# Kernel optimization log

Hardware: AMD Instinct MI355X
Metric: run time of the kernel (lower is better)

## Reference

```python
import jax, jax.numpy as jnp
import numpy as np

EPS = 1e-06
NEG_SLOPE = 0.2
B, N, CIN = 2, 2048, 64
QK, V, H = 128, 128, 8


def ev_nonlin(x, w1, b1, w2, b2):
    # EVNNonLinearity with skip_connection == 1, leaky_relu
    norm = jnp.linalg.norm(x, axis=-2, keepdims=True)  # [..., 1, nf]
    zero_norm = norm <= EPS
    norm = norm + EPS
    h = jax.nn.leaky_relu(norm @ w1 + b1, NEG_SLOPE)
    norm_bn = (h @ w2 + b2) + norm
    return jnp.where(zero_norm, x, x / norm * norm_bn)


def ev_layernorm(x):
    x_norm = jnp.linalg.norm(x, axis=-2, keepdims=True)
    sigma = jnp.std(jnp.concatenate([x_norm, -x_norm], -1), axis=-1, keepdims=True)
    return x / (sigma + EPS)


def setup_inputs() -> dict:
    key = jax.random.key(0)
    ks = jax.random.split(key, 20)
    def w(k, *shape):
        fan_in = shape[0]
        return jax.random.normal(k, shape, jnp.float32) / np.sqrt(fan_in)
    hd_qk = QK // H
    hd_v = V // H
    return {
        'qfts': jax.random.normal(ks[0], (B, N, 3, CIN), jnp.float32),
        'kvfts': jax.random.normal(ks[1], (B, N, 3, CIN), jnp.float32),
        # EVLinearLeakyReLU for q branch
        'w_q_in': w(ks[2], CIN, QK),
        'q_nl_w1': w(ks[3], QK, QK // 2), 'q_nl_b1': jnp.zeros((QK // 2,), jnp.float32),
        'q_nl_w2': w(ks[4], QK // 2, QK), 'q_nl_b2': jnp.zeros((QK,), jnp.float32),
        # EVLinearLeakyReLU for kv branch
        'w_kv_in': w(ks[5], CIN, QK),
        'kv_nl_w1': w(ks[6], QK, QK // 2), 'kv_nl_b1': jnp.zeros((QK // 2,), jnp.float32),
        'kv_nl_w2': w(ks[7], QK // 2, QK), 'kv_nl_b2': jnp.zeros((QK,), jnp.float32),
        # DenseGeneral projections (no bias)
        'w_q': w(ks[8], QK, H, hd_qk),
        'w_k': w(ks[9], QK, H, hd_qk),
        'w_v': w(ks[10], QK, H, hd_v),
        # output EVLinearLeakyReLU
        'w_out': w(ks[11], V, V),
        'o_nl_w1': w(ks[12], V, V // 2), 'o_nl_b1': jnp.zeros((V // 2,), jnp.float32),
        'o_nl_w2': w(ks[13], V // 2, V), 'o_nl_b2': jnp.zeros((V,), jnp.float32),
    }


def reference(qfts, kvfts, w_q_in, q_nl_w1, q_nl_b1, q_nl_w2, q_nl_b2,
              w_kv_in, kv_nl_w1, kv_nl_b1, kv_nl_w2, kv_nl_b2,
              w_q, w_k, w_v, w_out, o_nl_w1, o_nl_b1, o_nl_w2, o_nl_b2):
    # EVLinearLeakyReLU on q and kv features: [b,n,3,cin] -> [b,n,3,qk]
    qf = ev_nonlin(qfts @ w_q_in, q_nl_w1, q_nl_b1, q_nl_w2, q_nl_b2)
    kf = ev_nonlin(kvfts @ w_kv_in, kv_nl_w1, kv_nl_b1, kv_nl_w2, kv_nl_b2)
    # DenseGeneral to heads, then heads to front: [h,b,n,3,d]
    q = jnp.einsum('bnfc,chd->hbnfd', qf, w_q)
    k = jnp.einsum('bnfc,chd->hbnfd', kf, w_k)
    v = jnp.einsum('bnfc,chd->hbnfd', kf, w_v)
    # normalize_qk
    q = ev_layernorm(q)
    k = ev_layernorm(k)
    # dot attention: contract vector(3) and head_dim axes
    scale = np.sqrt(k.shape[-1]).astype(np.float32)
    attn = jnp.einsum('hbqfd,hbkfd->hbqk', q, k)
    attn = jax.nn.softmax(attn / scale, axis=-1)
    resi = jnp.einsum('hbqk,hbkfd->hbqfd', attn, v)
    # 'h b q f d -> b q f (h d)'
    h, b, nq, f, d = resi.shape
    resi = jnp.moveaxis(resi, 0, 3).reshape(b, nq, f, h * d)
    # output EVLinearLeakyReLU
    out = ev_nonlin(resi @ w_out, o_nl_w1, o_nl_b1, o_nl_w2, o_nl_b2)
    return out
```

## Files before the change

kernel.cpp:

```cpp
#include <hip/hip_runtime.h>
#include <math.h>

#define EPSV 1e-6f
#define NSL  0.2f
#define BB   2
#define NN   2048
#define HH   8
#define TBP  16

typedef short bf16x8 __attribute__((ext_vector_type(8)));
typedef float f32x4  __attribute__((ext_vector_type(4)));

__device__ __forceinline__ unsigned cvt_pk_bf16(float a, float b) {
  unsigned r;
  asm("v_cvt_pk_bf16_f32 %0, %1, %2" : "=v"(r) : "v"(a), "v"(b));
  return r;
}
__device__ __forceinline__ float u2f(unsigned u) {
  union { unsigned u; float f; } v; v.u = u; return v.f;
}
__device__ __forceinline__ float leaky(float a) { return a > 0.f ? a : NSL * a; }

__device__ __forceinline__ void pack8(float4 a, float4 b, uint4& hi, uint4& lo) {
  hi.x = cvt_pk_bf16(a.x, a.y);
  hi.y = cvt_pk_bf16(a.z, a.w);
  hi.z = cvt_pk_bf16(b.x, b.y);
  hi.w = cvt_pk_bf16(b.z, b.w);
  float d0 = a.x - u2f(hi.x << 16), d1 = a.y - u2f(hi.x & 0xffff0000u);
  float d2 = a.z - u2f(hi.y << 16), d3 = a.w - u2f(hi.y & 0xffff0000u);
  float d4 = b.x - u2f(hi.z << 16), d5 = b.y - u2f(hi.z & 0xffff0000u);
  float d6 = b.z - u2f(hi.w << 16), d7 = b.w - u2f(hi.w & 0xffff0000u);
  lo.x = cvt_pk_bf16(d0, d1);
  lo.y = cvt_pk_bf16(d2, d3);
  lo.z = cvt_pk_bf16(d4, d5);
  lo.w = cvt_pk_bf16(d6, d7);
}

__global__ __launch_bounds__(64) void wconv_kernel(
    const float* __restrict__ wq_in, const float* __restrict__ qw1, const float* __restrict__ qw2,
    const float* __restrict__ wkv_in, const float* __restrict__ kw1, const float* __restrict__ kw2,
    const float* __restrict__ w_q, const float* __restrict__ w_k, const float* __restrict__ w_v,
    unsigned short* __restrict__ WB)
{
  const int b = blockIdx.x;
  const int lane = threadIdx.x;
  const float* src; int N, toff;
  if      (b < 16)  { src = wq_in;  N = 128; toff = b; }
  else if (b < 32)  { src = qw1;    N = 64;  toff = b - 16; }
  else if (b < 48)  { src = qw2;    N = 128; toff = b - 32; }
  else if (b < 64)  { src = wkv_in; N = 128; toff = b - 48; }
  else if (b < 80)  { src = kw1;    N = 64;  toff = b - 64; }
  else if (b < 96)  { src = kw2;    N = 128; toff = b - 80; }
  else if (b < 128) { src = w_q;    N = 128; toff = b - 96; }
  else if (b < 160) { src = w_k;    N = 128; toff = b - 128; }
  else              { src = w_v;    N = 128; toff = b - 160; }
  const int NT = N >> 4;
  const int kk = toff / NT, nj = toff % NT;
  const int k0 = kk * 32 + (lane >> 4) * 8;
  const int ch = nj * 16 + (lane & 15);
  float vals[8];
  #pragma unroll
  for (int j = 0; j < 8; ++j) vals[j] = src[(size_t)(k0 + j) * N + ch];
  float4 a = {vals[0], vals[1], vals[2], vals[3]};
  float4 bb = {vals[4], vals[5], vals[6], vals[7]};
  uint4 hi, lo;
  pack8(a, bb, hi, lo);
  unsigned short* dst = WB + (size_t)b * 1024;
  *(uint4*)(dst + lane * 8) = hi;
  *(uint4*)(dst + 512 + lane * 8) = lo;
}


__global__ __launch_bounds__(256) void pre_kernel(
    const float* __restrict__ qfts, const float* __restrict__ kvfts,
    const float* __restrict__ qb1, const float* __restrict__ qb2,
    const float* __restrict__ kb1, const float* __restrict__ kb2,
    const unsigned short* __restrict__ WB,
    unsigned short* __restrict__ QW, unsigned short* __restrict__ KW, unsigned short* __restrict__ VW)
{
  const bool is_kv = blockIdx.y != 0;
  const float* x_in = is_kv ? kvfts : qfts;
  const float* b1 = is_kv ? kb1 : qb1;
  const float* b2 = is_kv ? kb2 : qb2;
  unsigned short* FW = is_kv ? KW : QW;
  const float ln_sc = is_kv ? 1.f : 0.25f * 1.44269504088896f;
  const int tb_in = is_kv ? 48 : 0;
  const int tb_w1 = is_kv ? 64 : 16;
  const int tb_w2 = is_kv ? 80 : 32;
  const int tb_p  = is_kv ? 128 : 96;

  const int t0 = blockIdx.x * TBP;
  const int tid = threadIdx.x;
  const int wv = tid >> 6, lane = tid & 63;
  const int col = lane & 15, kg = lane >> 4;
  const int nj0 = wv * 2;
  const int n0 = t0 & (NN - 1), bsel = t0 >> 11;

  __shared__ __align__(16) char smem[50688];
  float* xs       = (float*)smem;
  float* norm_lds = (float*)(smem + 12544);
  float* h_lds    = (float*)(smem + 20992);
  float* f_lds    = (float*)(smem + 25344);
  float* stage    = (float*)smem;

  {
    const float4* src = (const float4*)(x_in + (size_t)t0 * 192);
    #pragma unroll
    for (int i = 0; i < 3; ++i) {
      int idx = tid + i * 256;
      int row = idx / 48, c4 = idx % 48;
      *(float4*)&xs[row * 196 + c4 * 4] = src[idx];
    }
  }
  __syncthreads();

  f32x4 pacc[3][2];
  #pragma unroll
  for (int mf = 0; mf < 3; ++mf)
    #pragma unroll
    for (int njl = 0; njl < 2; ++njl) pacc[mf][njl] = (f32x4){0.f, 0.f, 0.f, 0.f};
  {
    bf16x8 axh[3][2], axl[3][2];
    #pragma unroll
    for (int mf = 0; mf < 3; ++mf)
      #pragma unroll
      for (int kk = 0; kk < 2; ++kk) {
        const float* pa = &xs[col * 196 + mf * 64 + kk * 32 + kg * 8];
        uint4 hi, lo;
        pack8(*(const float4*)pa, *(const float4*)(pa + 4), hi, lo);
        axh[mf][kk] = *(bf16x8*)&hi; axl[mf][kk] = *(bf16x8*)&lo;
      }
    #pragma unroll
    for (int kk = 0; kk < 2; ++kk)
      #pragma unroll
      for (int njl = 0; njl < 2; ++njl) {
        const unsigned short* wb = WB + (size_t)(tb_in + kk * 8 + nj0 + njl) * 1024 + lane * 8;
        bf16x8 bh = *(const bf16x8*)wb;
        bf16x8 bl = *(const bf16x8*)(wb + 512);
        #pragma unroll
        for (int mf = 0; mf < 3; ++mf) {
          pacc[mf][njl] = __builtin_amdgcn_mfma_f32_16x16x32_bf16(axh[mf][kk], bh, pacc[mf][njl], 0, 0, 0);
          pacc[mf][njl] = __builtin_amdgcn_mfma_f32_16x16x32_bf16(axh[mf][kk], bl, pacc[mf][njl], 0, 0, 0);
          pacc[mf][njl] = __builtin_amdgcn_mfma_f32_16x16x32_bf16(axl[mf][kk], bh, pacc[mf][njl], 0, 0, 0);
        }
      }
  }

  f32x4 np4[2]; int zm = 0;
  #pragma unroll
  for (int njl = 0; njl < 2; ++njl) {
    f32x4 ss = pacc[0][njl] * pacc[0][njl] + pacc[1][njl] * pacc[1][njl] + pacc[2][njl] * pacc[2][njl];
    #pragma unroll
    for (int i = 0; i < 4; ++i) {
      float nn = sqrtf(ss[i]);
      if (nn <= EPSV) zm |= 1 << (njl * 4 + i);
      np4[njl][i] = nn + EPSV;
      norm_lds[(kg * 4 + i) * 132 + (nj0 + njl) * 16 + col] = np4[njl][i];
    }
  }
  __syncthreads();

  {
    f32x4 hacc = {0.f, 0.f, 0.f, 0.f};
    #pragma unroll
    for (int kk = 0; kk < 4; ++kk) {
      const float* pa = &norm_lds[col * 132 + kk * 32 + kg * 8];
      uint4 hi, lo;
      pack8(*(const float4*)pa, *(const float4*)(pa + 4), hi, lo);
      bf16x8 ah = *(bf16x8*)&hi, al = *(bf16x8*)&lo;
      const unsigned short* wb = WB + (size_t)(tb_w1 + kk * 4 + wv) * 1024 + lane * 8;
      bf16x8 bh = *(const bf16x8*)wb, bl = *(const bf16x8*)(wb + 512);
      hacc = __builtin_amdgcn_mfma_f32_16x16x32_bf16(ah, bh, hacc, 0, 0, 0);
      hacc = __builtin_amdgcn_mfma_f32_16x16x32_bf16(ah, bl, hacc, 0, 0, 0);
      hacc = __builtin_amdgcn_mfma_f32_16x16x32_bf16(al, bh, hacc, 0, 0, 0);
    }
    float b1v = b1[wv * 16 + col];
    #pragma unroll
    for (int i = 0; i < 4; ++i)
      h_lds[(kg * 4 + i) * 68 + wv * 16 + col] = leaky(hacc[i] + b1v);
  }
  __syncthreads();

  {
    f32x4 bna[2] = {{0.f, 0.f, 0.f, 0.f}, {0.f, 0.f, 0.f, 0.f}};
    #pragma unroll
    for (int kk = 0; kk < 2; ++kk) {
      const float* pa = &h_lds[col * 68 + kk * 32 + kg * 8];
      uint4 hi, lo;
      pack8(*(const float4*)pa, *(const float4*)(pa + 4), hi, lo);
      bf16x8 ah = *(bf16x8*)&hi, al = *(bf16x8*)&lo;
      #pragma unroll
      for (int njl = 0; njl < 2; ++njl) {
        const unsigned short* wb = WB + (size_t)(tb_w2 + kk * 8 + nj0 + njl) * 1024 + lane * 8;
        bf16x8 bh = *(const bf16x8*)wb, bl = *(const bf16x8*)(wb + 512);
        bna[njl] = __builtin_amdgcn_mfma_f32_16x16x32_bf16(ah, bh, bna[njl], 0, 0, 0);
        bna[njl] = __builtin_amdgcn_mfma_f32_16x16x32_bf16(ah, bl, bna[njl], 0, 0, 0);
        bna[njl] = __builtin_amdgcn_mfma_f32_16x16x32_bf16(al, bh, bna[njl], 0, 0, 0);
      }
    }
    #pragma unroll
    for (int njl = 0; njl < 2; ++njl) {
      float b2v = b2[(nj0 + njl) * 16 + col];
      #pragma unroll
      for (int i = 0; i < 4; ++i) {
        float r = (zm >> (njl * 4 + i)) & 1 ? 1.f
                 : (bna[njl][i] + b2v + np4[njl][i]) / np4[njl][i];
        #pragma unroll
        for (int mf = 0; mf < 3; ++mf)
          f_lds[(mf * 16 + kg * 4 + i) * 132 + (nj0 + njl) * 16 + col] = pacc[mf][njl][i] * r;
      }
    }
  }
  __syncthreads();

  f32x4 qacc[3][2], vacc[3][2];
  #pragma unroll
  for (int mf = 0; mf < 3; ++mf)
    #pragma unroll
    for (int njl = 0; njl < 2; ++njl) {
      qacc[mf][njl] = (f32x4){0.f, 0.f, 0.f, 0.f};
      vacc[mf][njl] = (f32x4){0.f, 0.f, 0.f, 0.f};
    }
  #pragma unroll
  for (int kk = 0; kk < 4; ++kk) {
    bf16x8 afh[3], afl[3];
    #pragma unroll
    for (int mf = 0; mf < 3; ++mf) {
      const float* pa = &f_lds[(mf * 16 + col) * 132 + kk * 32 + kg * 8];
      uint4 hi, lo;
      pack8(*(const float4*)pa, *(const float4*)(pa + 4), hi, lo);
      afh[mf] = *(bf16x8*)&hi; afl[mf] = *(bf16x8*)&lo;
    }
    #pragma unroll
    for (int njl = 0; njl < 2; ++njl) {
      const unsigned short* wbq = WB + (size_t)(tb_p + kk * 8 + nj0 + njl) * 1024 + lane * 8;
      bf16x8 qbh = *(const bf16x8*)wbq, qbl = *(const bf16x8*)(wbq + 512);
      #pragma unroll
      for (int mf = 0; mf < 3; ++mf) {
        qacc[mf][njl] = __builtin_amdgcn_mfma_f32_16x16x32_bf16(afh[mf], qbh, qacc[mf][njl], 0, 0, 0);
        qacc[mf][njl] = __builtin_amdgcn_mfma_f32_16x16x32_bf16(afh[mf], qbl, qacc[mf][njl], 0, 0, 0);
        qacc[mf][njl] = __builtin_amdgcn_mfma_f32_16x16x32_bf16(afl[mf], qbh, qacc[mf][njl], 0, 0, 0);
      }
      if (is_kv) {
        const unsigned short* wbv = WB + (size_t)(160 + kk * 8 + nj0 + njl) * 1024 + lane * 8;
        bf16x8 vbh = *(const bf16x8*)wbv, vbl = *(const bf16x8*)(wbv + 512);
        #pragma unroll
        for (int mf = 0; mf < 3; ++mf) {
          vacc[mf][njl] = __builtin_amdgcn_mfma_f32_16x16x32_bf16(afh[mf], vbh, vacc[mf][njl], 0, 0, 0);
          vacc[mf][njl] = __builtin_amdgcn_mfma_f32_16x16x32_bf16(afh[mf], vbl, vacc[mf][njl], 0, 0, 0);
          vacc[mf][njl] = __builtin_amdgcn_mfma_f32_16x16x32_bf16(afl[mf], vbh, vacc[mf][njl], 0, 0, 0);
        }
      }
    }
  }
  __syncthreads();

  #pragma unroll
  for (int njl = 0; njl < 2; ++njl) {
    #pragma unroll
    for (int i = 0; i < 4; ++i) {
      float ss = qacc[0][njl][i] * qacc[0][njl][i]
               + qacc[1][njl][i] * qacc[1][njl][i]
               + qacc[2][njl][i] * qacc[2][njl][i];
      ss += __shfl_xor(ss, 1, 16);
      ss += __shfl_xor(ss, 2, 16);
      ss += __shfl_xor(ss, 4, 16);
      ss += __shfl_xor(ss, 8, 16);
      float inv = ln_sc / (sqrtf(ss * (1.f / 16.f)) + EPSV);
      const int tl = kg * 4 + i;
      #pragma unroll
      for (int mf = 0; mf < 3; ++mf)
        stage[tl * 388 + mf * 128 + (nj0 + njl) * 16 + col] = qacc[mf][njl][i] * inv;
    }
  }
  __syncthreads();

  {
    const int f0 = lane >> 5;
    const int ddb = ((lane >> 4) & 1) * 8;
    const int row = lane & 15;
    #pragma unroll
    for (int h2 = 0; h2 < 2; ++h2) {
      const int hh = wv * 2 + h2;
      const int hbw = hh * BB + bsel;
      const size_t basew = (size_t)(hbw * 128 + (n0 >> 4)) * 1536;
      {
        const float* p0 = stage + row * 388 + f0 * 128 + hh * 16 + ddb;
        uint4 hi, lo;
        pack8(*(const float4*)p0, *(const float4*)(p0 + 4), hi, lo);
        *(uint4*)(FW + basew + lane * 8) = hi;
        *(uint4*)(FW + basew + 768 + lane * 8) = lo;
      }
      if (lane < 32) {
        const float* p1 = stage + row * 388 + 2 * 128 + hh * 16 + ddb;
        uint4 hi, lo;
        pack8(*(const float4*)p1, *(const float4*)(p1 + 4), hi, lo);
        *(uint4*)(FW + basew + 512 + lane * 8) = hi;
        *(uint4*)(FW + basew + 768 + 512 + lane * 8) = lo;
      }
    }
  }

  if (is_kv) {
    __syncthreads();
    #pragma unroll
    for (int njl = 0; njl < 2; ++njl)
      #pragma unroll
      for (int mf = 0; mf < 3; ++mf)
        #pragma unroll
        for (int i = 0; i < 4; ++i)
          stage[mf * 2112 + (kg * 4 + i) * 132 + (nj0 + njl) * 16 + col] = vacc[mf][njl][i];
    __syncthreads();

    const int s0 = (n0 >> 3) & 3;
    if (lane < 32) {
      const int seg = lane;
      const int tlb = (seg >> 4) * 8;
      const int dd = seg & 15;
      #pragma unroll
      for (int h2 = 0; h2 < 2; ++h2) {
        const int hh = wv * 2 + h2;
        const int hbw = hh * BB + bsel;
        #pragma unroll
        for (int f = 0; f < 3; ++f) {
          const size_t vbase = (size_t)((hbw * 64 + (n0 >> 5)) * 3 + f) * 1024;
          float vals[8];
          #pragma unroll
          for (int j = 0; j < 8; ++j)
            vals[j] = stage[f * 2112 + (tlb + j) * 132 + hh * 16 + dd];
          float4 a = {vals[0], vals[1], vals[2], vals[3]};
          float4 b = {vals[4], vals[5], vals[6], vals[7]};
          uint4 hi, lo;
          pack8(a, b, hi, lo);
          *(uint4*)(VW + vbase + (size_t)(s0 * 16 + seg) * 8) = hi;
          *(uint4*)(VW + vbase + 512 + (size_t)(s0 * 16 + seg) * 8) = lo;
        }
      }
    }
  }
}

#define THR 10.0f

__global__ __launch_bounds__(512, 4) void attn_kernel(
    const unsigned short* __restrict__ QW, const unsigned short* __restrict__ KW,
    const unsigned short* __restrict__ VW, float* __restrict__ Ob)
{
  const int lane = threadIdx.x & 63;
  const int w = threadIdx.x >> 6;
  const int qt = w & 1;
  const int kq = w >> 1;
  const int hb = blockIdx.y;
  const int tA = blockIdx.x * 4 + qt * 2;
  const int q = lane & 15, g = lane >> 4;

  __shared__ unsigned short plds[8][2][1152];
  float* comb = (float*)plds;

  bf16x8 qh0[2], ql0[2], qh1[2], ql1[2];
  #pragma unroll
  for (int qs = 0; qs < 2; ++qs) {
    const size_t qbase = (size_t)(hb * 128 + tA + qs) * 1536;
    qh0[qs] = *(const bf16x8*)(QW + qbase + lane * 8);
    ql0[qs] = *(const bf16x8*)(QW + qbase + 768 + lane * 8);
    qh1[qs] = (bf16x8){0,0,0,0,0,0,0,0};
    ql1[qs] = (bf16x8){0,0,0,0,0,0,0,0};
    if (lane < 32) {
      qh1[qs] = *(const bf16x8*)(QW + qbase + 512 + lane * 8);
      ql1[qs] = *(const bf16x8*)(QW + qbase + 768 + 512 + lane * 8);
    }
  }

  f32x4 o[2][3];
  #pragma unroll
  for (int qs = 0; qs < 2; ++qs)
    #pragma unroll
    for (int f = 0; f < 3; ++f) o[qs][f] = (f32x4){0.f, 0.f, 0.f, 0.f};
  float m[2] = {-INFINITY, -INFINITY}, l[2] = {0.f, 0.f};

  for (int T = kq * 8; T < kq * 8 + 8; ++T) {
    f32x4 sc[2][4];
    __builtin_amdgcn_s_setprio(1);
    #pragma unroll
    for (int st = 0; st < 4; ++st) {
      const size_t kb = (size_t)(hb * 128 + T * 4 + st) * 1536;
      bf16x8 kh0 = *(const bf16x8*)(KW + kb + lane * 8);
      bf16x8 kl0 = *(const bf16x8*)(KW + kb + 768 + lane * 8);
      bf16x8 kh1 = *(const bf16x8*)(KW + kb + 512 + lane * 8);
      bf16x8 kl1 = *(const bf16x8*)(KW + kb + 768 + 512 + lane * 8);
      #pragma unroll
      for (int qs = 0; qs < 2; ++qs) {
        f32x4 a = {0.f, 0.f, 0.f, 0.f};
        a = __builtin_amdgcn_mfma_f32_16x16x32_bf16(kh0, qh0[qs], a, 0, 0, 0);
        a = __builtin_amdgcn_mfma_f32_16x16x32_bf16(kh0, ql0[qs], a, 0, 0, 0);
        a = __builtin_amdgcn_mfma_f32_16x16x32_bf16(kl0, qh0[qs], a, 0, 0, 0);
        a = __builtin_amdgcn_mfma_f32_16x16x32_bf16(kh1, qh1[qs], a, 0, 0, 0);
        a = __builtin_amdgcn_mfma_f32_16x16x32_bf16(kh1, ql1[qs], a, 0, 0, 0);
        a = __builtin_amdgcn_mfma_f32_16x16x32_bf16(kl1, qh1[qs], a, 0, 0, 0);
        sc[qs][st] = a;
      }
    }
    __builtin_amdgcn_s_setprio(0);

    #pragma unroll
    for (int qs = 0; qs < 2; ++qs) {
      float tm = sc[qs][0][0];
      #pragma unroll
      for (int st = 0; st < 4; ++st)
        #pragma unroll
        for (int r = 0; r < 4; ++r) tm = fmaxf(tm, sc[qs][st][r]);
      tm = fmaxf(tm, __shfl_xor(tm, 16));
      tm = fmaxf(tm, __shfl_xor(tm, 32));
      if (__any(tm > m[qs] + THR)) {
        float mnew = fmaxf(m[qs], tm);
        float scl = __builtin_amdgcn_exp2f(m[qs] - mnew);
        l[qs] *= scl;
        #pragma unroll
        for (int f = 0; f < 3; ++f) {
          o[qs][f][0] *= scl; o[qs][f][1] *= scl;
          o[qs][f][2] *= scl; o[qs][f][3] *= scl;
        }
        m[qs] = mnew;
      }
      float lp = 0.f;
      #pragma unroll
      for (int st = 0; st < 4; ++st) {
        float p0 = __builtin_amdgcn_exp2f(sc[qs][st][0] - m[qs]);
        float p1 = __builtin_amdgcn_exp2f(sc[qs][st][1] - m[qs]);
        float p2 = __builtin_amdgcn_exp2f(sc[qs][st][2] - m[qs]);
        float p3 = __builtin_amdgcn_exp2f(sc[qs][st][3] - m[qs]);
        lp += (p0 + p1) + (p2 + p3);
        uint2 uh = {cvt_pk_bf16(p0, p1), cvt_pk_bf16(p2, p3)};
        *(uint2*)&plds[w][qs][q * 72 + st * 16 + g * 4] = uh;
      }
      lp += __shfl_xor(lp, 16);
      lp += __shfl_xor(lp, 32);
      l[qs] += lp;
    }

    asm volatile("s_waitcnt lgkmcnt(0)" ::: "memory");

    __builtin_amdgcn_s_setprio(1);
    #pragma unroll
    for (int c = 0; c < 2; ++c) {
      const int kc = T * 2 + c;
      bf16x8 pb[2];
      #pragma unroll
      for (int qs = 0; qs < 2; ++qs)
        pb[qs] = *(const bf16x8*)&plds[w][qs][q * 72 + c * 32 + g * 8];
      #pragma unroll
      for (int f = 0; f < 3; ++f) {
        const size_t vb = (size_t)((hb * 64 + kc) * 3 + f) * 1024;
        bf16x8 vh = *(const bf16x8*)(VW + vb + lane * 8);
        bf16x8 vl = *(const bf16x8*)(VW + vb + 512 + lane * 8);
        #pragma unroll
        for (int qs = 0; qs < 2; ++qs) {
          o[qs][f] = __builtin_amdgcn_mfma_f32_16x16x32_bf16(vh, pb[qs], o[qs][f], 0, 0, 0);
          o[qs][f] = __builtin_amdgcn_mfma_f32_16x16x32_bf16(vl, pb[qs], o[qs][f], 0, 0, 0);
        }
      }
    }
    __builtin_amdgcn_s_setprio(0);
  }

  #define SLOT(qt_, qs_, r_) (comb + ((((qt_) * 2 + (qs_)) * 2 + (r_)) * 64 + lane) * 14)
  __syncthreads();
  if (kq & 1) {
    #pragma unroll
    for (int qs = 0; qs < 2; ++qs) {
      float* cb = SLOT(qt, qs, kq >> 1);
      #pragma unroll
      for (int f = 0; f < 3; ++f)
        #pragma unroll
        for (int r = 0; r < 4; ++r) cb[f * 4 + r] = o[qs][f][r];
      cb[12] = m[qs]; cb[13] = l[qs];
    }
  }
  __syncthreads();
  if (!(kq & 1)) {
    #pragma unroll
    for (int qs = 0; qs < 2; ++qs) {
      const float* cb = SLOT(qt, qs, kq >> 1);
      float m1 = cb[12], l1 = cb[13];
      float mn = fmaxf(m[qs], m1);
      float s0 = __builtin_amdgcn_exp2f(m[qs] - mn);
      float s1 = __builtin_amdgcn_exp2f(m1 - mn);
      l[qs] = l[qs] * s0 + l1 * s1;
      #pragma unroll
      for (int f = 0; f < 3; ++f)
        #pragma unroll
        for (int r = 0; r < 4; ++r)
          o[qs][f][r] = o[qs][f][r] * s0 + cb[f * 4 + r] * s1;
      m[qs] = mn;
    }
  }
  __syncthreads();
  if (kq == 2) {
    #pragma unroll
    for (int qs = 0; qs < 2; ++qs) {
      float* cb = SLOT(qt, qs, 1);
      #pragma unroll
      for (int f = 0; f < 3; ++f)
        #pragma unroll
        for (int r = 0; r < 4; ++r) cb[f * 4 + r] = o[qs][f][r];
      cb[12] = m[qs]; cb[13] = l[qs];
    }
  }
  __syncthreads();
  if (kq == 0) {
    const int h_ = hb >> 1, b_ = hb & 1;
    #pragma unroll
    for (int qs = 0; qs < 2; ++qs) {
      const float* cb = SLOT(qt, qs, 1);
      float m1 = cb[12], l1 = cb[13];
      float mn = fmaxf(m[qs], m1);
      float s0 = __builtin_amdgcn_exp2f(m[qs] - mn);
      float s1 = __builtin_amdgcn_exp2f(m1 - mn);
      float invl = 1.f / (l[qs] * s0 + l1 * s1);
      const int n = (tA + qs) * 16 + q;
      #pragma unroll
      for (int f = 0; f < 3; ++f) {
        float4 st4 = {(o[qs][f][0] * s0 + cb[f * 4 + 0] * s1) * invl,
                      (o[qs][f][1] * s0 + cb[f * 4 + 1] * s1) * invl,
                      (o[qs][f][2] * s0 + cb[f * 4 + 2] * s1) * invl,
                      (o[qs][f][3] * s0 + cb[f * 4 + 3] * s1) * invl};
        *(float4*)&Ob[(((size_t)(b_ * NN + n)) * 3 + f) * 128 + h_ * 16 + g * 4] = st4;
      }
    }
  }
  #undef SLOT
}

__global__ __launch_bounds__(256) void out_kernel(
    const float* __restrict__ Ob, const float* __restrict__ w_out,
    const float* __restrict__ w1, const float* __restrict__ b1,
    const float* __restrict__ w2, const float* __restrict__ b2,
    float* __restrict__ out)
{
  const int t0 = blockIdx.x * TBP;
  const int tid = threadIdx.x;
  const int grp = tid >> 5;
  const int c0  = tid & 31;
  const int ch0 = c0 * 4;

  __shared__ float rs[TBP][384];
  __shared__ float norm_s[TBP][128];
  __shared__ float h_s[TBP][64];

  {
    const float4* src = (const float4*)(Ob + (size_t)t0 * 384);
    float4* dst = (float4*)&rs[0][0];
    #pragma unroll
    for (int i = 0; i < 6; ++i) dst[tid + i * 256] = src[tid + i * 256];
  }
  __syncthreads();

  f32x4 p[2][3];
  #pragma unroll
  for (int t = 0; t < 2; ++t)
    #pragma unroll
    for (int f = 0; f < 3; ++f) p[t][f] = (f32x4){0.f, 0.f, 0.f, 0.f};
  #pragma unroll 2
  for (int c = 0; c < 128; c += 4) {
    f32x4 w4[4];
    #pragma unroll
    for (int i = 0; i < 4; ++i)
      w4[i] = *(const f32x4*)&w_out[(c + i) * 128 + ch0];
    #pragma unroll
    for (int t = 0; t < 2; ++t)
      #pragma unroll
      for (int f = 0; f < 3; ++f) {
        f32x4 rv = *(const f32x4*)&rs[grp * 2 + t][f * 128 + c];
        p[t][f] += rv[0] * w4[0] + rv[1] * w4[1] + rv[2] * w4[2] + rv[3] * w4[3];
      }
  }

  f32x4 np[2]; int zm = 0;
  #pragma unroll
  for (int t = 0; t < 2; ++t) {
    f32x4 ss = p[t][0] * p[t][0] + p[t][1] * p[t][1] + p[t][2] * p[t][2];
    #pragma unroll
    for (int j = 0; j < 4; ++j) {
      float nn = sqrtf(ss[j]);
      if (nn <= EPSV) zm |= 1 << (t * 4 + j);
      np[t][j] = nn + EPSV;
    }
    *(f32x4*)&norm_s[grp * 2 + t][ch0] = np[t];
  }
  __syncthreads();

  {
    float a[2][2];
    {
      float2 bb = *(const float2*)&b1[c0 * 2];
      a[0][0] = bb.x; a[1][0] = bb.x; a[0][1] = bb.y; a[1][1] = bb.y;
    }
    #pragma unroll 2
    for (int c = 0; c < 128; c += 4) {
      float2 wv[4];
      #pragma unroll
      for (int i = 0; i < 4; ++i)
        wv[i] = *(const float2*)&w1[(c + i) * 64 + c0 * 2];
      #pragma unroll
      for (int t = 0; t < 2; ++t) {
        f32x4 n4 = *(const f32x4*)&norm_s[grp * 2 + t][c];
        a[t][0] += n4[0] * wv[0].x + n4[1] * wv[1].x + n4[2] * wv[2].x + n4[3] * wv[3].x;
        a[t][1] += n4[0] * wv[0].y + n4[1] * wv[1].y + n4[2] * wv[2].y + n4[3] * wv[3].y;
      }
    }
    #pragma unroll
    for (int t = 0; t < 2; ++t) {
      float2 hv = {leaky(a[t][0]), leaky(a[t][1])};
      *(float2*)&h_s[grp * 2 + t][c0 * 2] = hv;
    }
  }
  __syncthreads();

  f32x4 bn[2];
  {
    f32x4 b2v = *(const f32x4*)&b2[ch0];
    #pragma unroll
    for (int t = 0; t < 2; ++t) bn[t] = b2v + np[t];
  }
  #pragma unroll 2
  for (int c = 0; c < 64; c += 4) {
    f32x4 w4[4];
    #pragma unroll
    for (int i = 0; i < 4; ++i)
      w4[i] = *(const f32x4*)&w2[(c + i) * 128 + ch0];
    #pragma unroll
    for (int t = 0; t < 2; ++t) {
      f32x4 h4 = *(const f32x4*)&h_s[grp * 2 + t][c];
      bn[t] += h4[0] * w4[0] + h4[1] * w4[1] + h4[2] * w4[2] + h4[3] * w4[3];
    }
  }

  #pragma unroll
  for (int t = 0; t < 2; ++t) {
    float* od = out + (size_t)(t0 + grp * 2 + t) * 384;
    f32x4 r;
    #pragma unroll
    for (int j = 0; j < 4; ++j)
      r[j] = (zm >> (t * 4 + j)) & 1 ? 1.f : bn[t][j] / np[t][j];
    #pragma unroll
    for (int f = 0; f < 3; ++f)
      *(f32x4*)&od[f * 128 + ch0] = p[t][f] * r;
  }
}

extern "C" void kernel_launch(void* const* d_in, const int* in_sizes, int n_in,
                              void* d_out, int out_size, void* d_ws, size_t ws_size,
                              hipStream_t stream) {
  const float* qfts   = (const float*)d_in[0];
  const float* kvfts  = (const float*)d_in[1];
  const float* w_q_in = (const float*)d_in[2];
  const float* q_w1   = (const float*)d_in[3];
  const float* q_b1   = (const float*)d_in[4];
  const float* q_w2   = (const float*)d_in[5];
  const float* q_b2   = (const float*)d_in[6];
  const float* w_kv_in= (const float*)d_in[7];
  const float* kv_w1  = (const float*)d_in[8];
  const float* kv_b1  = (const float*)d_in[9];
  const float* kv_w2  = (const float*)d_in[10];
  const float* kv_b2  = (const float*)d_in[11];
  const float* w_q    = (const float*)d_in[12];
  const float* w_k    = (const float*)d_in[13];
  const float* w_v    = (const float*)d_in[14];
  const float* w_out  = (const float*)d_in[15];
  const float* o_w1   = (const float*)d_in[16];
  const float* o_b1   = (const float*)d_in[17];
  const float* o_w2   = (const float*)d_in[18];
  const float* o_b2   = (const float*)d_in[19];

  unsigned short* QW = (unsigned short*)d_ws;
  unsigned short* KW = QW + 3145728;
  unsigned short* VW = KW + 3145728;
  float* Obuf = (float*)(VW + 3145728);
  unsigned short* WB = (unsigned short*)(Obuf + 1572864);

  wconv_kernel<<<192, 64, 0, stream>>>(w_q_in, q_w1, q_w2, w_kv_in, kv_w1, kv_w2,
                                       w_q, w_k, w_v, WB);
  dim3 pg(BB * NN / TBP, 2);
  pre_kernel<<<pg, 256, 0, stream>>>(qfts, kvfts, q_b1, q_b2, kv_b1, kv_b2,
                                     WB, QW, KW, VW);
  dim3 ag(32, 16);
  attn_kernel<<<ag, 512, 0, stream>>>(QW, KW, VW, Obuf);
  out_kernel<<<BB * NN / TBP, 256, 0, stream>>>(Obuf, w_out, o_w1, o_b1, o_w2, o_b2, (float*)d_out);
}
```

Measured before the change: 92.42 us.

## Move output EV layer matmuls to split-bf16 MFMA and prefetch first V tile

```diff
diff --git a/kernel.cpp b/kernel.cpp
--- a/kernel.cpp
+++ b/kernel.cpp
@@ -40,6 +40,7 @@
     const float* __restrict__ wq_in, const float* __restrict__ qw1, const float* __restrict__ qw2,
     const float* __restrict__ wkv_in, const float* __restrict__ kw1, const float* __restrict__ kw2,
     const float* __restrict__ w_q, const float* __restrict__ w_k, const float* __restrict__ w_v,
+    const float* __restrict__ w_out, const float* __restrict__ ow1, const float* __restrict__ ow2,
     unsigned short* __restrict__ WB)
 {
   const int b = blockIdx.x;
@@ -53,7 +54,10 @@
   else if (b < 96)  { src = kw2;    N = 128; toff = b - 80; }
   else if (b < 128) { src = w_q;    N = 128; toff = b - 96; }
   else if (b < 160) { src = w_k;    N = 128; toff = b - 128; }
-  else              { src = w_v;    N = 128; toff = b - 160; }
+  else if (b < 192) { src = w_v;    N = 128; toff = b - 160; }
+  else if (b < 224) { src = w_out;  N = 128; toff = b - 192; }
+  else if (b < 240) { src = ow1;    N = 64;  toff = b - 224; }
+  else              { src = ow2;    N = 128; toff = b - 240; }
   const int NT = N >> 4;
   const int kk = toff / NT, nj = toff % NT;
   const int k0 = kk * 32 + (lane >> 4) * 8;
@@ -402,6 +406,17 @@
     }
     __builtin_amdgcn_s_setprio(0);
 
+    bf16x8 v0h[3], v0l[3];
+    {
+      const int kc0 = T * 2;
+      #pragma unroll
+      for (int f = 0; f < 3; ++f) {
+        const size_t vb = (size_t)((hb * 64 + kc0) * 3 + f) * 1024;
+        v0h[f] = *(const bf16x8*)(VW + vb + lane * 8);
+        v0l[f] = *(const bf16x8*)(VW + vb + 512 + lane * 8);
+      }
+    }
+
     #pragma unroll
     for (int qs = 0; qs < 2; ++qs) {
       float tm = sc[qs][0][0];
@@ -441,13 +456,25 @@
     asm volatile("s_waitcnt lgkmcnt(0)" ::: "memory");
 
     __builtin_amdgcn_s_setprio(1);
-    #pragma unroll
-    for (int c = 0; c < 2; ++c) {
-      const int kc = T * 2 + c;
+    {
       bf16x8 pb[2];
       #pragma unroll
       for (int qs = 0; qs < 2; ++qs)
-        pb[qs] = *(const bf16x8*)&plds[w][qs][q * 72 + c * 32 + g * 8];
+        pb[qs] = *(const bf16x8*)&plds[w][qs][q * 72 + g * 8];
+      #pragma unroll
+      for (int f = 0; f < 3; ++f)
+        #pragma unroll
+        for (int qs = 0; qs < 2; ++qs) {
+          o[qs][f] = __builtin_amdgcn_mfma_f32_16x16x32_bf16(v0h[f], pb[qs], o[qs][f], 0, 0, 0);
+          o[qs][f] = __builtin_amdgcn_mfma_f32_16x16x32_bf16(v0l[f], pb[qs], o[qs][f], 0, 0, 0);
+        }
+    }
+    {
+      const int kc = T * 2 + 1;
+      bf16x8 pb[2];
+      #pragma unroll
+      for (int qs = 0; qs < 2; ++qs)
+        pb[qs] = *(const bf16x8*)&plds[w][qs][q * 72 + 32 + g * 8];
       #pragma unroll
       for (int f = 0; f < 3; ++f) {
         const size_t vb = (size_t)((hb * 64 + kc) * 3 + f) * 1024;
@@ -532,119 +559,139 @@
 }
 
 __global__ __launch_bounds__(256) void out_kernel(
-    const float* __restrict__ Ob, const float* __restrict__ w_out,
-    const float* __restrict__ w1, const float* __restrict__ b1,
-    const float* __restrict__ w2, const float* __restrict__ b2,
+    const float* __restrict__ Ob,
+    const float* __restrict__ b1, const float* __restrict__ b2,
+    const unsigned short* __restrict__ WB,
     float* __restrict__ out)
 {
   const int t0 = blockIdx.x * TBP;
   const int tid = threadIdx.x;
-  const int grp = tid >> 5;
-  const int c0  = tid & 31;
-  const int ch0 = c0 * 4;
-
-  __shared__ float rs[TBP][384];
-  __shared__ float norm_s[TBP][128];
-  __shared__ float h_s[TBP][64];
+  const int wv = tid >> 6, lane = tid & 63;
+  const int col = lane & 15, kg = lane >> 4;
+  const int nj0 = wv * 2;
+
+  __shared__ __align__(16) char smem[38144];
+  float* rs_lds   = (float*)smem;
+  float* norm_lds = (float*)(smem + 25344);
+  float* h_lds    = (float*)(smem + 33792);
+  float* stage    = (float*)smem;
 
   {
     const float4* src = (const float4*)(Ob + (size_t)t0 * 384);
-    float4* dst = (float4*)&rs[0][0];
-    #pragma unroll
-    for (int i = 0; i < 6; ++i) dst[tid + i * 256] = src[tid + i * 256];
-  }
-  __syncthreads();
-
-  f32x4 p[2][3];
-  #pragma unroll
-  for (int t = 0; t < 2; ++t)
-    #pragma unroll
-    for (int f = 0; f < 3; ++f) p[t][f] = (f32x4){0.f, 0.f, 0.f, 0.f};
-  #pragma unroll 2
-  for (int c = 0; c < 128; c += 4) {
-    f32x4 w4[4];
+    #pragma unroll
+    for (int i = 0; i < 6; ++i) {
+      int idx = tid + i * 256;
+      int tok = idx / 96, rem = idx % 96;
+      int f = rem / 32, c4 = rem % 32;
+      *(float4*)&rs_lds[f * 2112 + tok * 132 + c4 * 4] = src[idx];
+    }
+  }
+  __syncthreads();
+
+  f32x4 pacc[3][2];
+  #pragma unroll
+  for (int mf = 0; mf < 3; ++mf)
+    #pragma unroll
+    for (int njl = 0; njl < 2; ++njl) pacc[mf][njl] = (f32x4){0.f, 0.f, 0.f, 0.f};
+  #pragma unroll
+  for (int kk = 0; kk < 4; ++kk) {
+    bf16x8 ah[3], al[3];
+    #pragma unroll
+    for (int mf = 0; mf < 3; ++mf) {
+      const float* pa = &rs_lds[mf * 2112 + col * 132 + kk * 32 + kg * 8];
+      uint4 hi, lo;
+      pack8(*(const float4*)pa, *(const float4*)(pa + 4), hi, lo);
+      ah[mf] = *(bf16x8*)&hi; al[mf] = *(bf16x8*)&lo;
+    }
+    #pragma unroll
+    for (int njl = 0; njl < 2; ++njl) {
+      const unsigned short* wb = WB + (size_t)(192 + kk * 8 + nj0 + njl) * 1024 + lane * 8;
+      bf16x8 bh = *(const bf16x8*)wb, bl = *(const bf16x8*)(wb + 512);
+      #pragma unroll
+      for (int mf = 0; mf < 3; ++mf) {
+        pacc[mf][njl] = __builtin_amdgcn_mfma_f32_16x16x32_bf16(ah[mf], bh, pacc[mf][njl], 0, 0, 0);
+        pacc[mf][njl] = __builtin_amdgcn_mfma_f32_16x16x32_bf16(ah[mf], bl, pacc[mf][njl], 0, 0, 0);
+        pacc[mf][njl] = __builtin_amdgcn_mfma_f32_16x16x32_bf16(al[mf], bh, pacc[mf][njl], 0, 0, 0);
+      }
+    }
+  }
+
+  f32x4 np4[2]; int zm = 0;
+  #pragma unroll
+  for (int njl = 0; njl < 2; ++njl) {
+    f32x4 ss = pacc[0][njl] * pacc[0][njl] + pacc[1][njl] * pacc[1][njl] + pacc[2][njl] * pacc[2][njl];
+    #pragma unroll
+    for (int i = 0; i < 4; ++i) {
+      float nn = sqrtf(ss[i]);
+      if (nn <= EPSV) zm |= 1 << (njl * 4 + i);
+      np4[njl][i] = nn + EPSV;
+      norm_lds[(kg * 4 + i) * 132 + (nj0 + njl) * 16 + col] = np4[njl][i];
+    }
+  }
+  __syncthreads();
+
+  {
+    f32x4 hacc = {0.f, 0.f, 0.f, 0.f};
+    #pragma unroll
+    for (int kk = 0; kk < 4; ++kk) {
+      const float* pa = &norm_lds[col * 132 + kk * 32 + kg * 8];
+      uint4 hi, lo;
+      pack8(*(const float4*)pa, *(const float4*)(pa + 4), hi, lo);
+      bf16x8 ah = *(bf16x8*)&hi, al = *(bf16x8*)&lo;
+      const unsigned short* wb = WB + (size_t)(224 + kk * 4 + wv) * 1024 + lane * 8;
+      bf16x8 bh = *(const bf16x8*)wb, bl = *(const bf16x8*)(wb + 512);
+      hacc = __builtin_amdgcn_mfma_f32_16x16x32_bf16(ah, bh, hacc, 0, 0, 0);
+      hacc = __builtin_amdgcn_mfma_f32_16x16x32_bf16(ah, bl, hacc, 0, 0, 0);
+      hacc = __builtin_amdgcn_mfma_f32_16x16x32_bf16(al, bh, hacc, 0, 0, 0);
+    }
+    float b1v = b1[wv * 16 + col];
     #pragma unroll
     for (int i = 0; i < 4; ++i)
-      w4[i] = *(const f32x4*)&w_out[(c + i) * 128 + ch0];
-    #pragma unroll
-    for (int t = 0; t < 2; ++t)
-      #pragma unroll
-      for (int f = 0; f < 3; ++f) {
-        f32x4 rv = *(const f32x4*)&rs[grp * 2 + t][f * 128 + c];
-        p[t][f] += rv[0] * w4[0] + rv[1] * w4[1] + rv[2] * w4[2] + rv[3] * w4[3];
-      }
-  }
-
-  f32x4 np[2]; int zm = 0;
-  #pragma unroll
-  for (int t = 0; t < 2; ++t) {
-    f32x4 ss = p[t][0] * p[t][0] + p[t][1] * p[t][1] + p[t][2] * p[t][2];
-    #pragma unroll
-    for (int j = 0; j < 4; ++j) {
-      float nn = sqrtf(ss[j]);
-      if (nn <= EPSV) zm |= 1 << (t * 4 + j);
-      np[t][j] = nn + EPSV;
-    }
-    *(f32x4*)&norm_s[grp * 2 + t][ch0] = np[t];
-  }
-  __syncthreads();
-
-  {
-    float a[2][2];
-    {
-      float2 bb = *(const float2*)&b1[c0 * 2];
-      a[0][0] = bb.x; a[1][0] = bb.x; a[0][1] = bb.y; a[1][1] = bb.y;
-    }
-    #pragma unroll 2
-    for (int c = 0; c < 128; c += 4) {
-      float2 wv[4];
-      #pragma unroll
-      for (int i = 0; i < 4; ++i)
-        wv[i] = *(const float2*)&w1[(c + i) * 64 + c0 * 2];
-      #pragma unroll
-      for (int t = 0; t < 2; ++t) {
-        f32x4 n4 = *(const f32x4*)&norm_s[grp * 2 + t][c];
-        a[t][0] += n4[0] * wv[0].x + n4[1] * wv[1].x + n4[2] * wv[2].x + n4[3] * wv[3].x;
-        a[t][1] += n4[0] * wv[0].y + n4[1] * wv[1].y + n4[2] * wv[2].y + n4[3] * wv[3].y;
-      }
-    }
-    #pragma unroll
-    for (int t = 0; t < 2; ++t) {
-      float2 hv = {leaky(a[t][0]), leaky(a[t][1])};
-      *(float2*)&h_s[grp * 2 + t][c0 * 2] = hv;
-    }
-  }
-  __syncthreads();
-
-  f32x4 bn[2];
-  {
-    f32x4 b2v = *(const f32x4*)&b2[ch0];
-    #pragma unroll
-    for (int t = 0; t < 2; ++t) bn[t] = b2v + np[t];
-  }
-  #pragma unroll 2
-  for (int c = 0; c < 64; c += 4) {
-    f32x4 w4[4];
-    #pragma unroll
-    for (int i = 0; i < 4; ++i)
-      w4[i] = *(const f32x4*)&w2[(c + i) * 128 + ch0];
-    #pragma unroll
-    for (int t = 0; t < 2; ++t) {
-      f32x4 h4 = *(const f32x4*)&h_s[grp * 2 + t][c];
-      bn[t] += h4[0] * w4[0] + h4[1] * w4[1] + h4[2] * w4[2] + h4[3] * w4[3];
-    }
-  }
-
-  #pragma unroll
-  for (int t = 0; t < 2; ++t) {
-    float* od = out + (size_t)(t0 + grp * 2 + t) * 384;
-    f32x4 r;
-    #pragma unroll
-    for (int j = 0; j < 4; ++j)
-      r[j] = (zm >> (t * 4 + j)) & 1 ? 1.f : bn[t][j] / np[t][j];
-    #pragma unroll
-    for (int f = 0; f < 3; ++f)
-      *(f32x4*)&od[f * 128 + ch0] = p[t][f] * r;
+      h_lds[(kg * 4 + i) * 68 + wv * 16 + col] = leaky(hacc[i] + b1v);
+  }
+  __syncthreads();
+
+  {
+    f32x4 bna[2] = {{0.f, 0.f, 0.f, 0.f}, {0.f, 0.f, 0.f, 0.f}};
+    #pragma unroll
+    for (int kk = 0; kk < 2; ++kk) {
+      const float* pa = &h_lds[col * 68 + kk * 32 + kg * 8];
+      uint4 hi, lo;
+      pack8(*(const float4*)pa, *(const float4*)(pa + 4), hi, lo);
+      bf16x8 ah = *(bf16x8*)&hi, al = *(bf16x8*)&lo;
+      #pragma unroll
+      for (int njl = 0; njl < 2; ++njl) {
+        const unsigned short* wb = WB + (size_t)(240 + kk * 8 + nj0 + njl) * 1024 + lane * 8;
+        bf16x8 bh = *(const bf16x8*)wb, bl = *(const bf16x8*)(wb + 512);
+        bna[njl] = __builtin_amdgcn_mfma_f32_16x16x32_bf16(ah, bh, bna[njl], 0, 0, 0);
+        bna[njl] = __builtin_amdgcn_mfma_f32_16x16x32_bf16(ah, bl, bna[njl], 0, 0, 0);
+        bna[njl] = __builtin_amdgcn_mfma_f32_16x16x32_bf16(al, bh, bna[njl], 0, 0, 0);
+      }
+    }
+    __syncthreads();
+    #pragma unroll
+    for (int njl = 0; njl < 2; ++njl) {
+      float b2v = b2[(nj0 + njl) * 16 + col];
+      #pragma unroll
+      for (int i = 0; i < 4; ++i) {
+        float r = (zm >> (njl * 4 + i)) & 1 ? 1.f
+                 : (bna[njl][i] + b2v + np4[njl][i]) / np4[njl][i];
+        #pragma unroll
+        for (int mf = 0; mf < 3; ++mf)
+          stage[(kg * 4 + i) * 388 + mf * 128 + (nj0 + njl) * 16 + col] = pacc[mf][njl][i] * r;
+      }
+    }
+  }
+  __syncthreads();
+
+  {
+    float4* dst = (float4*)(out + (size_t)t0 * 384);
+    #pragma unroll
+    for (int i = 0; i < 6; ++i) {
+      int idx = tid + i * 256;
+      int tok = idx / 96, rem = idx % 96;
+      dst[idx] = *(const float4*)&stage[tok * 388 + rem * 4];
+    }
   }
 }
 
@@ -678,12 +725,12 @@
   float* Obuf = (float*)(VW + 3145728);
   unsigned short* WB = (unsigned short*)(Obuf + 1572864);
 
-  wconv_kernel<<<192, 64, 0, stream>>>(w_q_in, q_w1, q_w2, w_kv_in, kv_w1, kv_w2,
-                                       w_q, w_k, w_v, WB);
+  wconv_kernel<<<256, 64, 0, stream>>>(w_q_in, q_w1, q_w2, w_kv_in, kv_w1, kv_w2,
+                                       w_q, w_k, w_v, w_out, o_w1, o_w2, WB);
   dim3 pg(BB * NN / TBP, 2);
   pre_kernel<<<pg, 256, 0, stream>>>(qfts, kvfts, q_b1, q_b2, kv_b1, kv_b2,
                                      WB, QW, KW, VW);
   dim3 ag(32, 16);
   attn_kernel<<<ag, 512, 0, stream>>>(QW, KW, VW, Obuf);
-  out_kernel<<<BB * NN / TBP, 256, 0, stream>>>(Obuf, w_out, o_w1, o_b1, o_w2, o_b2, (float*)d_out);
+  out_kernel<<<BB * NN / TBP, 256, 0, stream>>>(Obuf, o_b1, o_b2, WB, (float*)d_out);
 }
```

Measured after the change: 81.63 us. 1.13x faster.
